# Kernel tuning notes

Hardware: AMD Instinct MI355X
Metric: run time of the kernel (lower is better)

Reference implementation:

```python
import jax, jax.numpy as jnp
import numpy as np

CTX = 768   # ctx_len in the original module
C = 768     # n_embd
B = 16
T = 768
K_EPS = 1e-8


def setup_inputs() -> dict:
    key = jax.random.key(0)
    ks = jax.random.split(key, 10)
    scale = 1.0 / np.sqrt(C)
    x = jax.random.normal(ks[0], (B, T, C), jnp.float32)
    time_decay = jax.random.normal(ks[1], (C, 1), jnp.float32) * 0.1
    time_first = jnp.full((C, 1), np.log(0.3), jnp.float32)
    time_mix_k = jax.random.uniform(ks[2], (1, 1, C), jnp.float32)
    time_mix_v = jax.random.uniform(ks[3], (1, 1, C), jnp.float32)
    time_mix_r = jax.random.uniform(ks[4], (1, 1, C), jnp.float32)
    Wk = jax.random.normal(ks[5], (C, C), jnp.float32) * scale
    Wv = jax.random.normal(ks[6], (C, C), jnp.float32) * scale
    Wr = jax.random.normal(ks[7], (C, C), jnp.float32) * scale
    Wo = jax.random.normal(ks[8], (C, C), jnp.float32) * scale
    return {"x": x, "time_decay": time_decay, "time_first": time_first,
            "time_mix_k": time_mix_k, "time_mix_v": time_mix_v, "time_mix_r": time_mix_r,
            "Wk": Wk, "Wv": Wv, "Wr": Wr, "Wo": Wo}


def reference(x, time_decay, time_first, time_mix_k, time_mix_v, time_mix_r, Wk, Wv, Wr, Wo):
    Bb, Tt, Cc = x.shape
    # time_shift: xx[t] = x[t-1], xx[0] = 0
    xx = jnp.pad(x, ((0, 0), (1, 0), (0, 0)))[:, :Tt]
    xk = x * time_mix_k + xx * (1.0 - time_mix_k)
    xv = x * time_mix_v + xx * (1.0 - time_mix_v)
    xr = x * time_mix_r + xx * (1.0 - time_mix_r)
    # projections (nn.Linear, no bias: y = x @ W.T); k, v laid out [B, C, T]
    k = jnp.einsum('btc,oc->bot', xk, Wk)
    v = jnp.einsum('btc,oc->bot', xv, Wv)
    r = jnp.einsum('btc,oc->bto', xr, Wr)
    k = jnp.exp(jnp.minimum(k, 60.0))
    kv = k * v
    # decay kernel: time_w = cat([exp(time_decay)*time_curve, time_first]); w = exp(time_w)[:, -T:]
    curve = (jnp.arange(CTX - 1) - (CTX - 2)).astype(x.dtype)  # [-(CTX-2) .. 0]
    tw = jnp.concatenate([jnp.exp(time_decay) * curve[None, :], time_first], axis=-1)  # [C, CTX]
    w = jnp.exp(tw)[:, -Tt:]            # [C, T]
    kern = w[:, None, :]                # [C, 1, T] depthwise kernel

    def causal_conv(z):  # z: [B, C, T] -> [B, C, T], left-padded cross-correlation
        return jax.lax.conv_general_dilated(
            z, kern, window_strides=(1,), padding=[(Tt - 1, 0)],
            feature_group_count=Cc, dimension_numbers=('NCH', 'OIH', 'NCH'))

    wkv = causal_conv(kv)
    wk = causal_conv(k) + K_EPS
    rwkv = jax.nn.sigmoid(r) * jnp.transpose(wkv / wk, (0, 2, 1))  # [B, T, C]
    return jnp.einsum('btc,oc->bto', rwkv, Wo)
```

## Files before the change

### kernel.cpp

```cpp
#include <hip/hip_runtime.h>
#include <math.h>

#define Mq 12288
#define Nq 768
#define Kq 768
#define Tq 768
#define Bq 16
#define Cq 768
#define BK 32

typedef __bf16 bf16x8 __attribute__((ext_vector_type(8)));
typedef __bf16 bf16x4 __attribute__((ext_vector_type(4)));
typedef float  floatx4 __attribute__((ext_vector_type(4)));

#define GLD_LDS16(g, l) __builtin_amdgcn_global_load_lds(                      \
    (const __attribute__((address_space(1))) unsigned int*)(g),                \
    (__attribute__((address_space(3))) unsigned int*)(l), 16, 0, 0)

__global__ __launch_bounds__(256)
void prep_w(const float* __restrict__ Wk, const float* __restrict__ Wv,
            const float* __restrict__ Wr, const float* __restrict__ Wo,
            __bf16* __restrict__ o)
{
    const int i   = blockIdx.x * 256 + threadIdx.x;
    const int a   = i / 147456;
    const int off = (i - a * 147456) * 4;
    const float* s = (a == 0) ? Wk : (a == 1) ? Wv : (a == 2) ? Wr : Wo;
    const float4 v = *(const float4*)(s + off);
    bf16x4 r = { (__bf16)v.x, (__bf16)v.y, (__bf16)v.z, (__bf16)v.w };
    *(bf16x4*)(o + (size_t)a * 589824 + off) = r;
}

__global__ __launch_bounds__(256)
void prep_mix(const float* __restrict__ x,
              const float* __restrict__ mk, const float* __restrict__ mv,
              const float* __restrict__ mr,
              __bf16* __restrict__ xk, __bf16* __restrict__ xv,
              __bf16* __restrict__ xr)
{
    const int i  = blockIdx.x * 256 + threadIdx.x;
    const int c4 = i % (Cq / 4);
    const int m  = i / (Cq / 4);
    const int t  = m % Tq;
    const int c0 = c4 * 4;

    const float4 xc = *(const float4*)(x + (size_t)m * Cq + c0);
    float4 xp = make_float4(0.f, 0.f, 0.f, 0.f);
    if (t > 0) xp = *(const float4*)(x + (size_t)(m - 1) * Cq + c0);

    const float4 k4 = *(const float4*)(mk + c0);
    const float4 v4 = *(const float4*)(mv + c0);
    const float4 r4 = *(const float4*)(mr + c0);

    bf16x4 ok = { (__bf16)fmaf(k4.x, xc.x - xp.x, xp.x),
                  (__bf16)fmaf(k4.y, xc.y - xp.y, xp.y),
                  (__bf16)fmaf(k4.z, xc.z - xp.z, xp.z),
                  (__bf16)fmaf(k4.w, xc.w - xp.w, xp.w) };
    bf16x4 ov = { (__bf16)fmaf(v4.x, xc.x - xp.x, xp.x),
                  (__bf16)fmaf(v4.y, xc.y - xp.y, xp.y),
                  (__bf16)fmaf(v4.z, xc.z - xp.z, xp.z),
                  (__bf16)fmaf(v4.w, xc.w - xp.w, xp.w) };
    bf16x4 orr = { (__bf16)fmaf(r4.x, xc.x - xp.x, xp.x),
                   (__bf16)fmaf(r4.y, xc.y - xp.y, xp.y),
                   (__bf16)fmaf(r4.z, xc.z - xp.z, xp.z),
                   (__bf16)fmaf(r4.w, xc.w - xp.w, xp.w) };
    const size_t o = (size_t)m * Cq + c0;
    *(bf16x4*)(xk + o) = ok;
    *(bf16x4*)(xv + o) = ov;
    *(bf16x4*)(xr + o) = orr;
}

template<int MODE, typename OutT>
__global__ __launch_bounds__(256)
void mfma_gemm(const __bf16* __restrict__ A,
               const __bf16* __restrict__ W,
               OutT* __restrict__ OUT)
{
    __shared__ __bf16 As[128 * BK];
    __shared__ __bf16 Bs[128 * BK];

    const int tid  = threadIdx.x;
    const int wave = tid >> 6;
    const int lane = tid & 63;
    const int m0   = blockIdx.y * 128;
    const int n0   = blockIdx.x * 128;

    const int r0  = wave * 32 + (lane >> 2);
    const int kc  = (lane & 3) ^ (r0 & 3);
    const __bf16* gA0 = A + (size_t)(m0 + r0) * Kq + kc * 8;
    const __bf16* gA1 = gA0 + (size_t)16 * Kq;
    const __bf16* gB0 = W + (size_t)(n0 + r0) * Kq + kc * 8;
    const __bf16* gB1 = gB0 + (size_t)16 * Kq;
    __bf16* lA0 = As + (wave * 2 + 0) * 512;
    __bf16* lA1 = As + (wave * 2 + 1) * 512;
    __bf16* lB0 = Bs + (wave * 2 + 0) * 512;
    __bf16* lB1 = Bs + (wave * 2 + 1) * 512;

    const int qr = wave >> 1, qc = wave & 1;
    const int rowA = qr * 64 + (lane & 15);
    const int rowB = qc * 64 + (lane & 15);
    const int lk   = lane >> 4;
    const int offA = (lk ^ (rowA & 3)) * 8;
    const int offB = (lk ^ (rowB & 3)) * 8;

    floatx4 acc[4][4];
#pragma unroll
    for (int i = 0; i < 4; ++i)
#pragma unroll
        for (int j = 0; j < 4; ++j) acc[i][j] = (floatx4){0.f, 0.f, 0.f, 0.f};

    for (int kt = 0; kt < Kq / BK; ++kt) {
        GLD_LDS16(gA0, lA0);
        GLD_LDS16(gA1, lA1);
        GLD_LDS16(gB0, lB0);
        GLD_LDS16(gB1, lB1);
        gA0 += BK; gA1 += BK; gB0 += BK; gB1 += BK;
        __syncthreads();

        bf16x8 aF[4], bF[4];
#pragma unroll
        for (int i = 0; i < 4; ++i)
            aF[i] = *(const bf16x8*)(As + (rowA + i * 16) * BK + offA);
#pragma unroll
        for (int j = 0; j < 4; ++j)
            bF[j] = *(const bf16x8*)(Bs + (rowB + j * 16) * BK + offB);

#pragma unroll
        for (int i = 0; i < 4; ++i)
#pragma unroll
            for (int j = 0; j < 4; ++j)
                acc[i][j] = __builtin_amdgcn_mfma_f32_16x16x32_bf16(
                    aF[i], bF[j], acc[i][j], 0, 0, 0);
        __syncthreads();
    }

    const int er = qr * 64 + (lane >> 4) * 4;
    const int ec = qc * 64 + (lane & 15);
#pragma unroll
    for (int i = 0; i < 4; ++i) {
#pragma unroll
        for (int j = 0; j < 4; ++j) {
            const int n = n0 + ec + j * 16;
#pragma unroll
            for (int reg = 0; reg < 4; ++reg) {
                const int m = m0 + er + i * 16 + reg;
                float v = acc[i][j][reg];
                if (MODE == 0)      v = expf(fminf(v, 60.f));
                else if (MODE == 2) v = 1.f / (1.f + expf(-v));
                OUT[(size_t)m * Nq + n] = (OutT)v;
            }
        }
    }
}

#define SEG 8
#define SLEN (Tq / SEG)

__global__ __launch_bounds__(512)
void scan_kernel(const __bf16* __restrict__ kb, const __bf16* __restrict__ vb,
                 __bf16* rb,
                 const float* __restrict__ td, const float* __restrict__ tf)
{
    __shared__ float aS[SEG][64];
    __shared__ float bS[SEG][64];

    const int cx  = threadIdx.x;
    const int seg = threadIdx.y;
    const int c   = blockIdx.x * 64 + cx;
    const int b   = blockIdx.y;

    const float d  = expf(td[c]);
    const float wd = expf(-d);
    const float u  = expf(tf[c]);

    const size_t base = ((size_t)b * Tq + seg * SLEN) * Cq + c;

    float a = 0.f, bs = 0.f;
    for (int t = 0; t < SLEN; ++t) {
        const size_t idx = base + (size_t)t * Cq;
        const float kt = (float)kb[idx];
        const float vt = (float)vb[idx];
        a  = fmaf(wd, a, kt * vt);
        bs = fmaf(wd, bs, kt);
    }
    aS[seg][cx] = a;
    bS[seg][cx] = bs;
    __syncthreads();

    if (seg == 0) {
        const float w96 = expf(-d * (float)SLEN);
        float ina = 0.f, inb = 0.f;
#pragma unroll
        for (int s = 0; s < SEG; ++s) {
            const float ta = aS[s][cx];
            const float tb = bS[s][cx];
            aS[s][cx] = ina;
            bS[s][cx] = inb;
            ina = fmaf(w96, ina, ta);
            inb = fmaf(w96, inb, tb);
        }
    }
    __syncthreads();

    a  = aS[seg][cx];
    bs = bS[seg][cx];
    for (int t = 0; t < SLEN; ++t) {
        const size_t idx = base + (size_t)t * Cq;
        const float kt = (float)kb[idx];
        const float vt = (float)vb[idx];
        const float sr = (float)rb[idx];
        const float kv = kt * vt;
        const float num = fmaf(u, kv, a);
        const float den = fmaf(u, kt, bs) + 1e-8f;
        rb[idx] = (__bf16)(sr * num / den);
        a  = fmaf(wd, a, kv);
        bs = fmaf(wd, bs, kt);
    }
}

extern "C" void kernel_launch(void* const* d_in, const int* in_sizes, int n_in,
                              void* d_out, int out_size, void* d_ws, size_t ws_size,
                              hipStream_t stream)
{
    const float* x  = (const float*)d_in[0];
    const float* td = (const float*)d_in[1];
    const float* tf = (const float*)d_in[2];
    const float* mk = (const float*)d_in[3];
    const float* mv = (const float*)d_in[4];
    const float* mr = (const float*)d_in[5];
    const float* Wk = (const float*)d_in[6];
    const float* Wv = (const float*)d_in[7];
    const float* Wr = (const float*)d_in[8];
    const float* Wo = (const float*)d_in[9];

    const size_t MC = (size_t)Mq * Cq;

    __bf16* xk = (__bf16*)d_out;
    __bf16* xv = xk + MC;

    __bf16* xr   = (__bf16*)d_ws;
    __bf16* kbuf = xr + MC;
    __bf16* vbuf = kbuf + MC;
    __bf16* rbuf = vbuf + MC;
    __bf16* Wp   = rbuf + MC;
    __bf16* Wkb = Wp;
    __bf16* Wvb = Wp + 589824;
    __bf16* Wrb = Wp + 2 * 589824;
    __bf16* Wob = Wp + 3 * 589824;

    prep_w<<<2304, 256, 0, stream>>>(Wk, Wv, Wr, Wo, Wp);
    prep_mix<<<(Mq * (Cq / 4)) / 256, 256, 0, stream>>>(x, mk, mv, mr, xk, xv, xr);

    const dim3 ggrid(Nq / 128, Mq / 128);
    mfma_gemm<0, __bf16><<<ggrid, 256, 0, stream>>>(xk, Wkb, kbuf);
    mfma_gemm<1, __bf16><<<ggrid, 256, 0, stream>>>(xv, Wvb, vbuf);
    mfma_gemm<2, __bf16><<<ggrid, 256, 0, stream>>>(xr, Wrb, rbuf);

    scan_kernel<<<dim3(Cq / 64, Bq), dim3(64, SEG), 0, stream>>>(
        kbuf, vbuf, rbuf, td, tf);

    mfma_gemm<3, float><<<ggrid, 256, 0, stream>>>(rbuf, Wob, (float*)d_out);
}
```

Baseline: 270.0 us.

## Batch K/V/R projections into one GEMM launch and deepen K tile to 64

```diff
diff --git a/kernel.cpp b/kernel.cpp
--- a/kernel.cpp
+++ b/kernel.cpp
@@ -7,7 +7,7 @@
 #define Tq 768
 #define Bq 16
 #define Cq 768
-#define BK 32
+#define BK 64
 
 typedef __bf16 bf16x8 __attribute__((ext_vector_type(8)));
 typedef __bf16 bf16x4 __attribute__((ext_vector_type(4)));
@@ -70,38 +70,48 @@
     *(bf16x4*)(xr + o) = orr;
 }
 
-template<int MODE, typename OutT>
+template<bool KVR>
 __global__ __launch_bounds__(256)
-void mfma_gemm(const __bf16* __restrict__ A,
+void mfma_gemm(const __bf16* __restrict__ A0, const __bf16* __restrict__ A1,
+               const __bf16* __restrict__ A2,
                const __bf16* __restrict__ W,
-               OutT* __restrict__ OUT)
+               __bf16* __restrict__ OUTb,
+               float*  __restrict__ OUTf)
 {
     __shared__ __bf16 As[128 * BK];
     __shared__ __bf16 Bs[128 * BK];
 
-    const int tid  = threadIdx.x;
-    const int wave = tid >> 6;
-    const int lane = tid & 63;
-    const int m0   = blockIdx.y * 128;
-    const int n0   = blockIdx.x * 128;
-
-    const int r0  = wave * 32 + (lane >> 2);
-    const int kc  = (lane & 3) ^ (r0 & 3);
-    const __bf16* gA0 = A + (size_t)(m0 + r0) * Kq + kc * 8;
-    const __bf16* gA1 = gA0 + (size_t)16 * Kq;
-    const __bf16* gB0 = W + (size_t)(n0 + r0) * Kq + kc * 8;
-    const __bf16* gB1 = gB0 + (size_t)16 * Kq;
-    __bf16* lA0 = As + (wave * 2 + 0) * 512;
-    __bf16* lA1 = As + (wave * 2 + 1) * 512;
-    __bf16* lB0 = Bs + (wave * 2 + 0) * 512;
-    __bf16* lB1 = Bs + (wave * 2 + 1) * 512;
+    const int tid   = threadIdx.x;
+    const int wave  = tid >> 6;
+    const int lane  = tid & 63;
+    const int m0    = blockIdx.y * 128;
+    const int nb    = blockIdx.x;
+    const int matid = KVR ? nb / 6 : 0;
+    const int n0    = KVR ? (nb % 6) * 128 : nb * 128;
+    const int wn0   = nb * 128;
+
+    const __bf16* A = KVR ? (matid == 0 ? A0 : matid == 1 ? A1 : A2) : A0;
+
+    const int r8 = lane >> 3;
+    const int cc = lane & 7;
+    const int sc = cc ^ r8;
+    const __bf16* gA[4];
+    const __bf16* gB[4];
+    __bf16* lA[4];
+    __bf16* lB[4];
+#pragma unroll
+    for (int i = 0; i < 4; ++i) {
+        const int row = (wave * 4 + i) * 8 + r8;
+        gA[i] = A + (size_t)(m0  + row) * Kq + sc * 8;
+        gB[i] = W + (size_t)(wn0 + row) * Kq + sc * 8;
+        lA[i] = As + (wave * 4 + i) * 512;
+        lB[i] = Bs + (wave * 4 + i) * 512;
+    }
 
     const int qr = wave >> 1, qc = wave & 1;
     const int rowA = qr * 64 + (lane & 15);
     const int rowB = qc * 64 + (lane & 15);
     const int lk   = lane >> 4;
-    const int offA = (lk ^ (rowA & 3)) * 8;
-    const int offB = (lk ^ (rowB & 3)) * 8;
 
     floatx4 acc[4][4];
 #pragma unroll
@@ -110,27 +120,36 @@
         for (int j = 0; j < 4; ++j) acc[i][j] = (floatx4){0.f, 0.f, 0.f, 0.f};
 
     for (int kt = 0; kt < Kq / BK; ++kt) {
-        GLD_LDS16(gA0, lA0);
-        GLD_LDS16(gA1, lA1);
-        GLD_LDS16(gB0, lB0);
-        GLD_LDS16(gB1, lB1);
-        gA0 += BK; gA1 += BK; gB0 += BK; gB1 += BK;
+#pragma unroll
+        for (int i = 0; i < 4; ++i) {
+            GLD_LDS16(gA[i], lA[i]);
+            GLD_LDS16(gB[i], lB[i]);
+            gA[i] += BK; gB[i] += BK;
+        }
         __syncthreads();
 
-        bf16x8 aF[4], bF[4];
-#pragma unroll
-        for (int i = 0; i < 4; ++i)
-            aF[i] = *(const bf16x8*)(As + (rowA + i * 16) * BK + offA);
-#pragma unroll
-        for (int j = 0; j < 4; ++j)
-            bF[j] = *(const bf16x8*)(Bs + (rowB + j * 16) * BK + offB);
-
-#pragma unroll
-        for (int i = 0; i < 4; ++i)
-#pragma unroll
-            for (int j = 0; j < 4; ++j)
-                acc[i][j] = __builtin_amdgcn_mfma_f32_16x16x32_bf16(
-                    aF[i], bF[j], acc[i][j], 0, 0, 0);
+#pragma unroll
+        for (int kk = 0; kk < 2; ++kk) {
+            bf16x8 aF[4], bF[4];
+#pragma unroll
+            for (int i = 0; i < 4; ++i) {
+                const int ra = rowA + i * 16;
+                aF[i] = *(const bf16x8*)(As + ra * BK +
+                                         (((kk << 2) | lk) ^ (ra & 7)) * 8);
+            }
+#pragma unroll
+            for (int j = 0; j < 4; ++j) {
+                const int rb = rowB + j * 16;
+                bF[j] = *(const bf16x8*)(Bs + rb * BK +
+                                         (((kk << 2) | lk) ^ (rb & 7)) * 8);
+            }
+#pragma unroll
+            for (int i = 0; i < 4; ++i)
+#pragma unroll
+                for (int j = 0; j < 4; ++j)
+                    acc[i][j] = __builtin_amdgcn_mfma_f32_16x16x32_bf16(
+                        aF[i], bF[j], acc[i][j], 0, 0, 0);
+        }
         __syncthreads();
     }
 
@@ -145,9 +164,13 @@
             for (int reg = 0; reg < 4; ++reg) {
                 const int m = m0 + er + i * 16 + reg;
                 float v = acc[i][j][reg];
-                if (MODE == 0)      v = expf(fminf(v, 60.f));
-                else if (MODE == 2) v = 1.f / (1.f + expf(-v));
-                OUT[(size_t)m * Nq + n] = (OutT)v;
+                if (KVR) {
+                    if (matid == 0)      v = expf(fminf(v, 60.f));
+                    else if (matid == 2) v = 1.f / (1.f + expf(-v));
+                    OUTb[(size_t)matid * Mq * Nq + (size_t)m * Nq + n] = (__bf16)v;
+                } else {
+                    OUTf[(size_t)m * Nq + n] = v;
+                }
             }
         }
     }
@@ -243,21 +266,17 @@
     __bf16* vbuf = kbuf + MC;
     __bf16* rbuf = vbuf + MC;
     __bf16* Wp   = rbuf + MC;
-    __bf16* Wkb = Wp;
-    __bf16* Wvb = Wp + 589824;
-    __bf16* Wrb = Wp + 2 * 589824;
-    __bf16* Wob = Wp + 3 * 589824;
+    __bf16* Wob  = Wp + 3 * 589824;
 
     prep_w<<<2304, 256, 0, stream>>>(Wk, Wv, Wr, Wo, Wp);
     prep_mix<<<(Mq * (Cq / 4)) / 256, 256, 0, stream>>>(x, mk, mv, mr, xk, xv, xr);
 
-    const dim3 ggrid(Nq / 128, Mq / 128);
-    mfma_gemm<0, __bf16><<<ggrid, 256, 0, stream>>>(xk, Wkb, kbuf);
-    mfma_gemm<1, __bf16><<<ggrid, 256, 0, stream>>>(xv, Wvb, vbuf);
-    mfma_gemm<2, __bf16><<<ggrid, 256, 0, stream>>>(xr, Wrb, rbuf);
+    mfma_gemm<true><<<dim3(18, 96), 256, 0, stream>>>(
+        xk, xv, xr, Wp, kbuf, nullptr);
 
     scan_kernel<<<dim3(Cq / 64, Bq), dim3(64, SEG), 0, stream>>>(
         kbuf, vbuf, rbuf, td, tf);
 
-    mfma_gemm<3, float><<<ggrid, 256, 0, stream>>>(rbuf, Wob, (float*)d_out);
-}
+    mfma_gemm<false><<<dim3(6, 96), 256, 0, stream>>>(
+        rbuf, nullptr, nullptr, Wob, nullptr, (float*)d_out);
+}
```

Measured after the change: 255.1 us. -5.5%, faster.
